# Performance work log

Hardware: AMD Instinct MI355X
Metric: run time of the kernel (lower is better)

## Reference

```python
import jax, jax.numpy as jnp
import numpy as np

N_MELS, HIDDEN, HEAD_DIM = 80, 128, 64


def _gru_step(h, gx_t, w_hh, b_hh):
    # PyTorch GRU cell math. gx_t = x_t @ W_ih^T + b_ih, precomputed. [B, 3H]
    H = h.shape[-1]
    gh = h @ w_hh.T + b_hh  # [B, 3H]
    r = jax.nn.sigmoid(gx_t[:, :H] + gh[:, :H])
    z = jax.nn.sigmoid(gx_t[:, H:2 * H] + gh[:, H:2 * H])
    n = jnp.tanh(gx_t[:, 2 * H:] + r * gh[:, 2 * H:])
    return (1.0 - z) * n + z * h


def setup_inputs() -> dict:
    key = jax.random.key(0)
    ks = jax.random.split(key, 14)
    s = 1.0 / np.sqrt(HIDDEN)
    u = lambda k, shape, sc: jax.random.uniform(k, shape, jnp.float32, -sc, sc)
    return {
        "x": jax.random.normal(ks[0], (128, 1500, N_MELS), dtype=jnp.float32),
        # forward-direction GRU params
        "w_ih_f": u(ks[1], (3 * HIDDEN, N_MELS), s),
        "w_hh_f": u(ks[2], (3 * HIDDEN, HIDDEN), s),
        "b_ih_f": u(ks[3], (3 * HIDDEN,), s),
        "b_hh_f": u(ks[4], (3 * HIDDEN,), s),
        # backward-direction GRU params
        "w_ih_b": u(ks[5], (3 * HIDDEN, N_MELS), s),
        "w_hh_b": u(ks[6], (3 * HIDDEN, HIDDEN), s),
        "b_ih_b": u(ks[7], (3 * HIDDEN,), s),
        "b_hh_b": u(ks[8], (3 * HIDDEN,), s),
        # MLP head: Linear(2H, 64) -> ReLU -> Linear(64, 1)
        "w1": u(ks[9], (HEAD_DIM, 2 * HIDDEN), 1.0 / np.sqrt(2 * HIDDEN)),
        "b1": u(ks[10], (HEAD_DIM,), 1.0 / np.sqrt(2 * HIDDEN)),
        "w2": u(ks[11], (1, HEAD_DIM), 1.0 / np.sqrt(HEAD_DIM)),
        "b2": u(ks[12], (1,), 1.0 / np.sqrt(HEAD_DIM)),
    }


def reference(x, w_ih_f, w_hh_f, b_ih_f, b_hh_f, w_ih_b, w_hh_b, b_ih_b, b_hh_b, w1, b1, w2, b2):
    B, T, _ = x.shape
    h0 = jnp.zeros((B, HIDDEN), dtype=x.dtype)

    # Forward direction: last output = final hidden state after full scan.
    # Precompute input projections for all timesteps in one GEMM.
    gx_f = jnp.einsum('bti,gi->tbg', x, w_ih_f) + b_ih_f  # [T, B, 3H]
    h_f, _ = jax.lax.scan(lambda h, g: (_gru_step(h, g, w_hh_f, b_hh_f), None), h0, gx_f)

    # Backward direction: out[:, -1, H:] in PyTorch is the backward hidden
    # after processing ONLY x[:, -1] (the reverse scan's first step), so a
    # single GRU step from h0 reproduces it exactly.
    gx_b_last = x[:, -1, :] @ w_ih_b.T + b_ih_b  # [B, 3H]
    h_b = _gru_step(h0, gx_b_last, w_hh_b, b_hh_b)

    last = jnp.concatenate([h_f, h_b], axis=-1)  # [B, 2H]
    # Head (eval mode: dropout is identity)
    hdn = jax.nn.relu(last @ w1.T + b1)
    out = hdn @ w2.T + b2  # [B, 1]
    return out[:, 0]
```

## Files before the change

kernel.cpp:

```cpp
#include <hip/hip_runtime.h>

#define B 128
#define T 1500
#define NI 80
#define H 128
#define G 384
#define TT 64

typedef float v2f __attribute__((ext_vector_type(2)));

__device__ __forceinline__ float sigf(float x) { return 1.0f / (1.0f + __expf(-x)); }
__device__ __forceinline__ float tanhfast(float x) { return 1.0f - 2.0f / (1.0f + __expf(2.0f * x)); }
__device__ __forceinline__ v2f pkfma(v2f a, v2f b, v2f c) { return __builtin_elementwise_fma(a, b, c); }

__device__ __forceinline__ float sum8(float v) {
    int a = __builtin_bit_cast(int, v);
    float m = __builtin_bit_cast(float, __builtin_amdgcn_update_dpp(0, a, 0x141, 0xF, 0xF, true));
    float s = v + m;
    a = __builtin_bit_cast(int, s);
    m = __builtin_bit_cast(float, __builtin_amdgcn_update_dpp(0, a, 0x1B, 0xF, 0xF, true));
    s = s + m;
    a = __builtin_bit_cast(int, s);
    m = __builtin_bit_cast(float, __builtin_amdgcn_update_dpp(0, a, 0xB1, 0xF, 0xF, true));
    return s + m;
}

__global__ __launch_bounds__(384)
void gx_gemm_kernel(const float* __restrict__ x, const float* __restrict__ w_ih,
                    const float* __restrict__ b_ih, float* __restrict__ gx,
                    int t0, int ct) {
    int tile = blockIdx.x;
    int b = blockIdx.y;
    int tl0 = tile * TT;
    if (tl0 >= ct) return;
    int n = (ct - tl0 < TT) ? (ct - tl0) : TT;
    int tid = threadIdx.x;

    __shared__ __align__(16) float xs[TT * NI];
    const float4* xsrc4 = (const float4*)(x + ((size_t)b * T + (size_t)(t0 + tl0)) * NI);
    int total4 = n * (NI / 4);
    for (int i = tid; i < total4; i += 384) ((float4*)xs)[i] = xsrc4[i];

    v2f w2[40];
    const v2f* wr = (const v2f*)(w_ih + (size_t)tid * NI);
#pragma unroll
    for (int i = 0; i < 40; ++i) w2[i] = wr[i];
    float bias = b_ih[tid];
    __syncthreads();

    float* gout = gx + ((size_t)b * ct + (size_t)tl0) * G + tid;
    int tt = 0;
    for (; tt + 2 <= n; tt += 2) {
        const float4* xa4 = (const float4*)(xs + tt * NI);
        const float4* xb4 = (const float4*)(xs + (tt + 1) * NI);
        v2f a0 = {0.f, 0.f}, a1 = {0.f, 0.f}, c0 = {0.f, 0.f}, c1 = {0.f, 0.f};
#pragma unroll
        for (int i = 0; i < 20; ++i) {
            float4 xa = xa4[i];
            float4 xb = xb4[i];
            v2f alo = {xa.x, xa.y}, ahi = {xa.z, xa.w};
            v2f blo = {xb.x, xb.y}, bhi = {xb.z, xb.w};
            a0 = pkfma(w2[2 * i], alo, a0);
            a1 = pkfma(w2[2 * i + 1], ahi, a1);
            c0 = pkfma(w2[2 * i], blo, c0);
            c1 = pkfma(w2[2 * i + 1], bhi, c1);
        }
        gout[(size_t)tt * G]       = bias + ((a0.x + a0.y) + (a1.x + a1.y));
        gout[(size_t)(tt + 1) * G] = bias + ((c0.x + c0.y) + (c1.x + c1.y));
    }
    if (tt < n) {
        const float4* xa4 = (const float4*)(xs + tt * NI);
        v2f a0 = {0.f, 0.f}, a1 = {0.f, 0.f};
#pragma unroll
        for (int i = 0; i < 20; ++i) {
            float4 xa = xa4[i];
            v2f alo = {xa.x, xa.y}, ahi = {xa.z, xa.w};
            a0 = pkfma(w2[2 * i], alo, a0);
            a1 = pkfma(w2[2 * i + 1], ahi, a1);
        }
        gout[(size_t)tt * G] = bias + ((a0.x + a0.y) + (a1.x + a1.y));
    }
}

__global__ __launch_bounds__(512)
void scan_kernel(const float* __restrict__ gx, const float* __restrict__ w_hh,
                 const float* __restrict__ b_hh, float* __restrict__ h_state,
                 int ct, int first, int last,
                 const float* __restrict__ x,
                 const float* __restrict__ w_ih_b, const float* __restrict__ b_ih_b,
                 const float* __restrict__ b_hh_b,
                 const float* __restrict__ w1, const float* __restrict__ b1,
                 const float* __restrict__ w2, const float* __restrict__ b2,
                 float* __restrict__ out) {
    int b = blockIdx.x;
    int tid = threadIdx.x;
    int jp = tid >> 3;
    int q = tid & 7;
    int j0 = jp, j1 = jp + 64;
    int jsel = (q < 4) ? j0 : j1;
    int hsel = ((jsel >> 4) * 20) + (jsel & 15);
    bool writer = (q & 3) == 0;

    __shared__ __align__(16) float hs[2][160];
    __shared__ __align__(16) float tail_gx[G];
    __shared__ __align__(16) float last_s[2 * H];
    __shared__ __align__(16) float xb_s[NI];

    float4 W0r[4], W0z[4], W0n[4], W1r[4], W1z[4], W1n[4];
    {
        const float* wb = w_hh + 16 * q;
        const float4* p0 = (const float4*)(wb + (size_t)j0 * H);
        const float4* p1 = (const float4*)(wb + (size_t)(j0 + H) * H);
        const float4* p2 = (const float4*)(wb + (size_t)(j0 + 2 * H) * H);
        const float4* p3 = (const float4*)(wb + (size_t)j1 * H);
        const float4* p4 = (const float4*)(wb + (size_t)(j1 + H) * H);
        const float4* p5 = (const float4*)(wb + (size_t)(j1 + 2 * H) * H);
#pragma unroll
        for (int i = 0; i < 4; ++i) {
            W0r[i] = p0[i]; W0z[i] = p1[i]; W0n[i] = p2[i];
            W1r[i] = p3[i]; W1z[i] = p4[i]; W1n[i] = p5[i];
        }
    }
    float br = b_hh[jsel], bz = b_hh[jsel + H], bn = b_hh[jsel + 2 * H];

    float h_cur = 0.f;
    if (!first) h_cur = h_state[b * H + jsel];
    if (writer) hs[0][hsel] = h_cur;

    float ga0, ga1, ga2, gb0 = 0.f, gb1 = 0.f, gb2 = 0.f;
    {
        const float* gp = gx + (size_t)b * ct * G;
        ga0 = gp[jsel]; ga1 = gp[jsel + H]; ga2 = gp[jsel + 2 * H];
        if (ct > 1) { gb0 = gp[G + jsel]; gb1 = gp[G + jsel + H]; gb2 = gp[G + jsel + 2 * H]; }
    }
    __syncthreads();

    auto step = [&](int TL, int SB, float& g0, float& g1, float& g2) {
        const float4* hv4 = (const float4*)(&hs[SB][0] + 20 * q);
        float4 h0 = hv4[0], h1 = hv4[1], h2 = hv4[2], h3 = hv4[3];
        v2f a0r = {0.f, 0.f}, a0z = {0.f, 0.f}, a0n = {0.f, 0.f};
        v2f a1r = {0.f, 0.f}, a1z = {0.f, 0.f}, a1n = {0.f, 0.f};
        v2f hl, hh;
        hl = v2f{h0.x, h0.y}; hh = v2f{h0.z, h0.w};
        a0r = pkfma(v2f{W0r[0].x, W0r[0].y}, hl, a0r); a0r = pkfma(v2f{W0r[0].z, W0r[0].w}, hh, a0r);
        a0z = pkfma(v2f{W0z[0].x, W0z[0].y}, hl, a0z); a0z = pkfma(v2f{W0z[0].z, W0z[0].w}, hh, a0z);
        a0n = pkfma(v2f{W0n[0].x, W0n[0].y}, hl, a0n); a0n = pkfma(v2f{W0n[0].z, W0n[0].w}, hh, a0n);
        a1r = pkfma(v2f{W1r[0].x, W1r[0].y}, hl, a1r); a1r = pkfma(v2f{W1r[0].z, W1r[0].w}, hh, a1r);
        a1z = pkfma(v2f{W1z[0].x, W1z[0].y}, hl, a1z); a1z = pkfma(v2f{W1z[0].z, W1z[0].w}, hh, a1z);
        a1n = pkfma(v2f{W1n[0].x, W1n[0].y}, hl, a1n); a1n = pkfma(v2f{W1n[0].z, W1n[0].w}, hh, a1n);
        hl = v2f{h1.x, h1.y}; hh = v2f{h1.z, h1.w};
        a0r = pkfma(v2f{W0r[1].x, W0r[1].y}, hl, a0r); a0r = pkfma(v2f{W0r[1].z, W0r[1].w}, hh, a0r);
        a0z = pkfma(v2f{W0z[1].x, W0z[1].y}, hl, a0z); a0z = pkfma(v2f{W0z[1].z, W0z[1].w}, hh, a0z);
        a0n = pkfma(v2f{W0n[1].x, W0n[1].y}, hl, a0n); a0n = pkfma(v2f{W0n[1].z, W0n[1].w}, hh, a0n);
        a1r = pkfma(v2f{W1r[1].x, W1r[1].y}, hl, a1r); a1r = pkfma(v2f{W1r[1].z, W1r[1].w}, hh, a1r);
        a1z = pkfma(v2f{W1z[1].x, W1z[1].y}, hl, a1z); a1z = pkfma(v2f{W1z[1].z, W1z[1].w}, hh, a1z);
        a1n = pkfma(v2f{W1n[1].x, W1n[1].y}, hl, a1n); a1n = pkfma(v2f{W1n[1].z, W1n[1].w}, hh, a1n);
        hl = v2f{h2.x, h2.y}; hh = v2f{h2.z, h2.w};
        a0r = pkfma(v2f{W0r[2].x, W0r[2].y}, hl, a0r); a0r = pkfma(v2f{W0r[2].z, W0r[2].w}, hh, a0r);
        a0z = pkfma(v2f{W0z[2].x, W0z[2].y}, hl, a0z); a0z = pkfma(v2f{W0z[2].z, W0z[2].w}, hh, a0z);
        a0n = pkfma(v2f{W0n[2].x, W0n[2].y}, hl, a0n); a0n = pkfma(v2f{W0n[2].z, W0n[2].w}, hh, a0n);
        a1r = pkfma(v2f{W1r[2].x, W1r[2].y}, hl, a1r); a1r = pkfma(v2f{W1r[2].z, W1r[2].w}, hh, a1r);
        a1z = pkfma(v2f{W1z[2].x, W1z[2].y}, hl, a1z); a1z = pkfma(v2f{W1z[2].z, W1z[2].w}, hh, a1z);
        a1n = pkfma(v2f{W1n[2].x, W1n[2].y}, hl, a1n); a1n = pkfma(v2f{W1n[2].z, W1n[2].w}, hh, a1n);
        hl = v2f{h3.x, h3.y}; hh = v2f{h3.z, h3.w};
        a0r = pkfma(v2f{W0r[3].x, W0r[3].y}, hl, a0r); a0r = pkfma(v2f{W0r[3].z, W0r[3].w}, hh, a0r);
        a0z = pkfma(v2f{W0z[3].x, W0z[3].y}, hl, a0z); a0z = pkfma(v2f{W0z[3].z, W0z[3].w}, hh, a0z);
        a0n = pkfma(v2f{W0n[3].x, W0n[3].y}, hl, a0n); a0n = pkfma(v2f{W0n[3].z, W0n[3].w}, hh, a0n);
        a1r = pkfma(v2f{W1r[3].x, W1r[3].y}, hl, a1r); a1r = pkfma(v2f{W1r[3].z, W1r[3].w}, hh, a1r);
        a1z = pkfma(v2f{W1z[3].x, W1z[3].y}, hl, a1z); a1z = pkfma(v2f{W1z[3].z, W1z[3].w}, hh, a1z);
        a1n = pkfma(v2f{W1n[3].x, W1n[3].y}, hl, a1n); a1n = pkfma(v2f{W1n[3].z, W1n[3].w}, hh, a1n);

        float s0r = sum8(a0r.x + a0r.y), s0z = sum8(a0z.x + a0z.y), s0n = sum8(a0n.x + a0n.y);
        float s1r = sum8(a1r.x + a1r.y), s1z = sum8(a1z.x + a1z.y), s1n = sum8(a1n.x + a1n.y);
        bool lo = q < 4;
        float ar = lo ? s0r : s1r;
        float az = lo ? s0z : s1z;
        float an = lo ? s0n : s1n;
        float r = sigf(g0 + br + ar);
        float z = sigf(g1 + bz + az);
        float n = tanhfast(g2 + r * (bn + an));
        h_cur = n + z * (h_cur - n);
        if (writer) hs[SB ^ 1][hsel] = h_cur;
        if (TL + 2 < ct) {
            const float* gp = gx + ((size_t)b * ct + TL + 2) * G;
            g0 = gp[jsel]; g1 = gp[jsel + H]; g2 = gp[jsel + 2 * H];
        }
        asm volatile("s_waitcnt lgkmcnt(0)\n\ts_barrier" ::: "memory");
    };

    int tl = 0;
    for (; tl + 1 < ct; tl += 2) {
        step(tl,     0, ga0, ga1, ga2);
        step(tl + 1, 1, gb0, gb1, gb2);
    }
    if (tl < ct) step(tl, 0, ga0, ga1, ga2);

    if (!last) {
        if (writer) h_state[b * H + jsel] = h_cur;
        return;
    }

    if (tid < NI) xb_s[tid] = x[((size_t)b * T + (T - 1)) * NI + tid];
    if (writer) last_s[jsel] = h_cur;
    __syncthreads();

    if (tid < G) {
        const float4* wbr = (const float4*)(w_ih_b + (size_t)tid * NI);
        const float4* xv = (const float4*)xb_s;
        float a0 = 0.f, a1 = 0.f, a2 = 0.f, a3 = 0.f;
#pragma unroll
        for (int i = 0; i < 20; ++i) {
            float4 wv = wbr[i]; float4 x4 = xv[i];
            a0 = fmaf(wv.x, x4.x, a0); a1 = fmaf(wv.y, x4.y, a1);
            a2 = fmaf(wv.z, x4.z, a2); a3 = fmaf(wv.w, x4.w, a3);
        }
        tail_gx[tid] = b_ih_b[tid] + ((a0 + a1) + (a2 + a3));
    }
    __syncthreads();

    if (tid < H) {
        float r = sigf(tail_gx[tid] + b_hh_b[tid]);
        float z = sigf(tail_gx[tid + H] + b_hh_b[tid + H]);
        float n = tanhfast(tail_gx[tid + 2 * H] + r * b_hh_b[tid + 2 * H]);
        last_s[H + tid] = (1.f - z) * n;
    }
    __syncthreads();

    if (tid < 64) {
        const float4* w1r = (const float4*)(w1 + (size_t)tid * 2 * H);
        const float4* lv = (const float4*)last_s;
        float a0 = 0.f, a1 = 0.f, a2 = 0.f, a3 = 0.f;
#pragma unroll
        for (int i = 0; i < 64; ++i) {
            float4 wv = w1r[i]; float4 l4 = lv[i];
            a0 = fmaf(wv.x, l4.x, a0); a1 = fmaf(wv.y, l4.y, a1);
            a2 = fmaf(wv.z, l4.z, a2); a3 = fmaf(wv.w, l4.w, a3);
        }
        float v = b1[tid] + ((a0 + a1) + (a2 + a3));
        v = fmaxf(v, 0.f) * w2[tid];
#pragma unroll
        for (int off = 32; off > 0; off >>= 1) v += __shfl_down(v, off);
        if (tid == 0) out[b] = v + b2[0];
    }
}

extern "C" void kernel_launch(void* const* d_in, const int* in_sizes, int n_in,
                              void* d_out, int out_size, void* d_ws, size_t ws_size,
                              hipStream_t stream) {
    (void)in_sizes; (void)n_in; (void)out_size;
    const float* x      = (const float*)d_in[0];
    const float* w_ih_f = (const float*)d_in[1];
    const float* w_hh_f = (const float*)d_in[2];
    const float* b_ih_f = (const float*)d_in[3];
    const float* b_hh_f = (const float*)d_in[4];
    const float* w_ih_b = (const float*)d_in[5];
    const float* w_hh_b = (const float*)d_in[6];
    const float* b_ih_b = (const float*)d_in[7];
    const float* b_hh_b = (const float*)d_in[8];
    const float* w1     = (const float*)d_in[9];
    const float* b1     = (const float*)d_in[10];
    const float* w2     = (const float*)d_in[11];
    const float* b2     = (const float*)d_in[12];
    (void)w_hh_b;
    float* out = (float*)d_out;

    float* h_state = (float*)d_ws;
    float* gxbuf = h_state + B * H;
    size_t hbytes = (size_t)B * H * sizeof(float);
    size_t avail = ws_size > hbytes ? ws_size - hbytes : 0;
    long long chunkT = (long long)(avail / ((size_t)B * G * sizeof(float)));
    if (chunkT > T) chunkT = T;
    if (chunkT < 1) chunkT = 1;

    for (int t0 = 0; t0 < T; t0 += (int)chunkT) {
        int ct = (T - t0 < (int)chunkT) ? (T - t0) : (int)chunkT;
        int ntiles = (ct + TT - 1) / TT;
        gx_gemm_kernel<<<dim3(ntiles, B), dim3(384), 0, stream>>>(
            x, w_ih_f, b_ih_f, gxbuf, t0, ct);
        scan_kernel<<<dim3(B), dim3(512), 0, stream>>>(
            gxbuf, w_hh_f, b_hh_f, h_state, ct,
            (t0 == 0) ? 1 : 0, (t0 + ct >= T) ? 1 : 0,
            x, w_ih_b, b_ih_b, b_hh_b, w1, b1, w2, b2, out);
    }
}
```

Before: 1.151 ms.

## Transpose gate-projection buffer, register-tile GEMM, prefetch four scan steps per load

The input-projection GEMM now writes gates as [B][G][T] instead of [B][T][G]. It is rewritten as a shared-memory tiled outer product: 64 gates by 128 timesteps per block, with each thread holding 4x8 accumulators. With the new layout the recurrent scan can fetch four consecutive timesteps per gate in one float4 load, prefetched a superstep ahead, which takes global loads off most serial steps. This requires chunk lengths to be multiples of 4, with clamped tail reads. It also adds register pressure from the launch-bounds occupancy hints.

Measured after the change: 1.209 ms. 5.0% more time.

```diff
diff --git a/kernel.cpp b/kernel.cpp
--- a/kernel.cpp
+++ b/kernel.cpp
@@ -5,7 +5,8 @@
 #define NI 80
 #define H 128
 #define G 384
-#define TT 64
+#define GT 64
+#define NTT 128
 
 typedef float v2f __attribute__((ext_vector_type(2)));
 
@@ -25,65 +26,81 @@
     return s + m;
 }
 
-__global__ __launch_bounds__(384)
+__global__ __launch_bounds__(256, 2)
 void gx_gemm_kernel(const float* __restrict__ x, const float* __restrict__ w_ih,
-                    const float* __restrict__ b_ih, float* __restrict__ gx,
+                    const float* __restrict__ b_ih, float* __restrict__ gxT,
                     int t0, int ct) {
-    int tile = blockIdx.x;
-    int b = blockIdx.y;
-    int tl0 = tile * TT;
-    if (tl0 >= ct) return;
-    int n = (ct - tl0 < TT) ? (ct - tl0) : TT;
+    __shared__ __align__(16) float wT[80][GT + 2];
+    __shared__ __align__(16) float xT[80][NTT + 4];
+    __shared__ float bias_s[GT];
     int tid = threadIdx.x;
-
-    __shared__ __align__(16) float xs[TT * NI];
-    const float4* xsrc4 = (const float4*)(x + ((size_t)b * T + (size_t)(t0 + tl0)) * NI);
-    int total4 = n * (NI / 4);
-    for (int i = tid; i < total4; i += 384) ((float4*)xs)[i] = xsrc4[i];
-
-    v2f w2[40];
-    const v2f* wr = (const v2f*)(w_ih + (size_t)tid * NI);
-#pragma unroll
-    for (int i = 0; i < 40; ++i) w2[i] = wr[i];
-    float bias = b_ih[tid];
-    __syncthreads();
-
-    float* gout = gx + ((size_t)b * ct + (size_t)tl0) * G + tid;
-    int tt = 0;
-    for (; tt + 2 <= n; tt += 2) {
-        const float4* xa4 = (const float4*)(xs + tt * NI);
-        const float4* xb4 = (const float4*)(xs + (tt + 1) * NI);
-        v2f a0 = {0.f, 0.f}, a1 = {0.f, 0.f}, c0 = {0.f, 0.f}, c1 = {0.f, 0.f};
-#pragma unroll
-        for (int i = 0; i < 20; ++i) {
-            float4 xa = xa4[i];
-            float4 xb = xb4[i];
-            v2f alo = {xa.x, xa.y}, ahi = {xa.z, xa.w};
-            v2f blo = {xb.x, xb.y}, bhi = {xb.z, xb.w};
-            a0 = pkfma(w2[2 * i], alo, a0);
-            a1 = pkfma(w2[2 * i + 1], ahi, a1);
-            c0 = pkfma(w2[2 * i], blo, c0);
-            c1 = pkfma(w2[2 * i + 1], bhi, c1);
-        }
-        gout[(size_t)tt * G]       = bias + ((a0.x + a0.y) + (a1.x + a1.y));
-        gout[(size_t)(tt + 1) * G] = bias + ((c0.x + c0.y) + (c1.x + c1.y));
-    }
-    if (tt < n) {
-        const float4* xa4 = (const float4*)(xs + tt * NI);
-        v2f a0 = {0.f, 0.f}, a1 = {0.f, 0.f};
-#pragma unroll
-        for (int i = 0; i < 20; ++i) {
-            float4 xa = xa4[i];
-            v2f alo = {xa.x, xa.y}, ahi = {xa.z, xa.w};
-            a0 = pkfma(w2[2 * i], alo, a0);
-            a1 = pkfma(w2[2 * i + 1], ahi, a1);
-        }
-        gout[(size_t)tt * G] = bias + ((a0.x + a0.y) + (a1.x + a1.y));
-    }
-}
-
-__global__ __launch_bounds__(512)
-void scan_kernel(const float* __restrict__ gx, const float* __restrict__ w_hh,
+    int b = blockIdx.z;
+    int g0b = blockIdx.y * GT;
+    int tt0 = blockIdx.x * NTT;
+
+    for (int i = tid; i < GT * 20; i += 256) {
+        int g = i & (GT - 1);
+        int kc = i >> 6;
+        float4 v = *(const float4*)(w_ih + (size_t)(g0b + g) * NI + 4 * kc);
+        wT[4 * kc + 0][g] = v.x; wT[4 * kc + 1][g] = v.y;
+        wT[4 * kc + 2][g] = v.z; wT[4 * kc + 3][g] = v.w;
+    }
+    for (int i = tid; i < NTT * 20; i += 256) {
+        int c = i & (NTT - 1);
+        int kc = i >> 7;
+        int tt = tt0 + c; if (tt > ct - 1) tt = ct - 1;
+        float4 v = *(const float4*)(x + ((size_t)b * T + (size_t)(t0 + tt)) * NI + 4 * kc);
+        xT[4 * kc + 0][c] = v.x; xT[4 * kc + 1][c] = v.y;
+        xT[4 * kc + 2][c] = v.z; xT[4 * kc + 3][c] = v.w;
+    }
+    if (tid < GT) bias_s[tid] = b_ih[g0b + tid];
+    __syncthreads();
+
+    int gi = tid & 15;
+    int ti = tid >> 4;
+    v2f acc[4][4];
+#pragma unroll
+    for (int r = 0; r < 4; ++r)
+#pragma unroll
+        for (int j = 0; j < 4; ++j) acc[r][j] = v2f{0.f, 0.f};
+
+#pragma unroll 2
+    for (int k = 0; k < 80; ++k) {
+        const v2f* wv = (const v2f*)&wT[k][4 * gi];
+        v2f w01 = wv[0], w23 = wv[1];
+        const float4* xv = (const float4*)&xT[k][8 * ti];
+        float4 x03 = xv[0], x47 = xv[1];
+        v2f xp0 = {x03.x, x03.y}, xp1 = {x03.z, x03.w};
+        v2f xp2 = {x47.x, x47.y}, xp3 = {x47.z, x47.w};
+        float wr[4] = {w01.x, w01.y, w23.x, w23.y};
+#pragma unroll
+        for (int r = 0; r < 4; ++r) {
+            v2f ws = {wr[r], wr[r]};
+            acc[r][0] = pkfma(ws, xp0, acc[r][0]);
+            acc[r][1] = pkfma(ws, xp1, acc[r][1]);
+            acc[r][2] = pkfma(ws, xp2, acc[r][2]);
+            acc[r][3] = pkfma(ws, xp3, acc[r][3]);
+        }
+    }
+
+#pragma unroll
+    for (int r = 0; r < 4; ++r) {
+        int g = g0b + 4 * gi + r;
+        float bias = bias_s[4 * gi + r];
+        float* orow = gxT + ((size_t)b * G + g) * ct + tt0 + 8 * ti;
+#pragma unroll
+        for (int j = 0; j < 4; ++j) {
+            int t = tt0 + 8 * ti + 2 * j;
+            if (t < ct) {
+                float2 o; o.x = acc[r][j].x + bias; o.y = acc[r][j].y + bias;
+                *(float2*)(orow + 2 * j) = o;
+            }
+        }
+    }
+}
+
+__global__ __launch_bounds__(512, 2)
+void scan_kernel(const float* __restrict__ gxT, const float* __restrict__ w_hh,
                  const float* __restrict__ b_hh, float* __restrict__ h_state,
                  int ct, int first, int last,
                  const float* __restrict__ x,
@@ -106,17 +123,17 @@
     __shared__ __align__(16) float last_s[2 * H];
     __shared__ __align__(16) float xb_s[NI];
 
-    float4 W0r[4], W0z[4], W0n[4], W1r[4], W1z[4], W1n[4];
+    v2f W0r[8], W0z[8], W0n[8], W1r[8], W1z[8], W1n[8];
     {
         const float* wb = w_hh + 16 * q;
-        const float4* p0 = (const float4*)(wb + (size_t)j0 * H);
-        const float4* p1 = (const float4*)(wb + (size_t)(j0 + H) * H);
-        const float4* p2 = (const float4*)(wb + (size_t)(j0 + 2 * H) * H);
-        const float4* p3 = (const float4*)(wb + (size_t)j1 * H);
-        const float4* p4 = (const float4*)(wb + (size_t)(j1 + H) * H);
-        const float4* p5 = (const float4*)(wb + (size_t)(j1 + 2 * H) * H);
-#pragma unroll
-        for (int i = 0; i < 4; ++i) {
+        const v2f* p0 = (const v2f*)(wb + (size_t)j0 * H);
+        const v2f* p1 = (const v2f*)(wb + (size_t)(j0 + H) * H);
+        const v2f* p2 = (const v2f*)(wb + (size_t)(j0 + 2 * H) * H);
+        const v2f* p3 = (const v2f*)(wb + (size_t)j1 * H);
+        const v2f* p4 = (const v2f*)(wb + (size_t)(j1 + H) * H);
+        const v2f* p5 = (const v2f*)(wb + (size_t)(j1 + 2 * H) * H);
+#pragma unroll
+        for (int i = 0; i < 8; ++i) {
             W0r[i] = p0[i]; W0z[i] = p1[i]; W0n[i] = p2[i];
             W1r[i] = p3[i]; W1z[i] = p4[i]; W1n[i] = p5[i];
         }
@@ -127,49 +144,34 @@
     if (!first) h_cur = h_state[b * H + jsel];
     if (writer) hs[0][hsel] = h_cur;
 
-    float ga0, ga1, ga2, gb0 = 0.f, gb1 = 0.f, gb2 = 0.f;
+    const float* gp0 = gxT + ((size_t)b * G + jsel) * ct;
+    const float* gp1 = gp0 + (size_t)H * ct;
+    const float* gp2 = gp0 + (size_t)(2 * H) * ct;
+
+    float4 A0, A1, A2, B0, B1, B2;
+    A0 = *(const float4*)(gp0); A1 = *(const float4*)(gp1); A2 = *(const float4*)(gp2);
     {
-        const float* gp = gx + (size_t)b * ct * G;
-        ga0 = gp[jsel]; ga1 = gp[jsel + H]; ga2 = gp[jsel + 2 * H];
-        if (ct > 1) { gb0 = gp[G + jsel]; gb1 = gp[G + jsel + H]; gb2 = gp[G + jsel + 2 * H]; }
-    }
-    __syncthreads();
-
-    auto step = [&](int TL, int SB, float& g0, float& g1, float& g2) {
-        const float4* hv4 = (const float4*)(&hs[SB][0] + 20 * q);
+        int t4 = (ct - 4 < 4) ? (ct - 4) : 4;
+        B0 = *(const float4*)(gp0 + t4); B1 = *(const float4*)(gp1 + t4); B2 = *(const float4*)(gp2 + t4);
+    }
+    __syncthreads();
+
+    auto dostep = [&](float g0, float g1, float g2, const float* SRC, float* DST) {
+        const float4* hv4 = (const float4*)(SRC + 20 * q);
         float4 h0 = hv4[0], h1 = hv4[1], h2 = hv4[2], h3 = hv4[3];
         v2f a0r = {0.f, 0.f}, a0z = {0.f, 0.f}, a0n = {0.f, 0.f};
         v2f a1r = {0.f, 0.f}, a1z = {0.f, 0.f}, a1n = {0.f, 0.f};
-        v2f hl, hh;
-        hl = v2f{h0.x, h0.y}; hh = v2f{h0.z, h0.w};
-        a0r = pkfma(v2f{W0r[0].x, W0r[0].y}, hl, a0r); a0r = pkfma(v2f{W0r[0].z, W0r[0].w}, hh, a0r);
-        a0z = pkfma(v2f{W0z[0].x, W0z[0].y}, hl, a0z); a0z = pkfma(v2f{W0z[0].z, W0z[0].w}, hh, a0z);
-        a0n = pkfma(v2f{W0n[0].x, W0n[0].y}, hl, a0n); a0n = pkfma(v2f{W0n[0].z, W0n[0].w}, hh, a0n);
-        a1r = pkfma(v2f{W1r[0].x, W1r[0].y}, hl, a1r); a1r = pkfma(v2f{W1r[0].z, W1r[0].w}, hh, a1r);
-        a1z = pkfma(v2f{W1z[0].x, W1z[0].y}, hl, a1z); a1z = pkfma(v2f{W1z[0].z, W1z[0].w}, hh, a1z);
-        a1n = pkfma(v2f{W1n[0].x, W1n[0].y}, hl, a1n); a1n = pkfma(v2f{W1n[0].z, W1n[0].w}, hh, a1n);
-        hl = v2f{h1.x, h1.y}; hh = v2f{h1.z, h1.w};
-        a0r = pkfma(v2f{W0r[1].x, W0r[1].y}, hl, a0r); a0r = pkfma(v2f{W0r[1].z, W0r[1].w}, hh, a0r);
-        a0z = pkfma(v2f{W0z[1].x, W0z[1].y}, hl, a0z); a0z = pkfma(v2f{W0z[1].z, W0z[1].w}, hh, a0z);
-        a0n = pkfma(v2f{W0n[1].x, W0n[1].y}, hl, a0n); a0n = pkfma(v2f{W0n[1].z, W0n[1].w}, hh, a0n);
-        a1r = pkfma(v2f{W1r[1].x, W1r[1].y}, hl, a1r); a1r = pkfma(v2f{W1r[1].z, W1r[1].w}, hh, a1r);
-        a1z = pkfma(v2f{W1z[1].x, W1z[1].y}, hl, a1z); a1z = pkfma(v2f{W1z[1].z, W1z[1].w}, hh, a1z);
-        a1n = pkfma(v2f{W1n[1].x, W1n[1].y}, hl, a1n); a1n = pkfma(v2f{W1n[1].z, W1n[1].w}, hh, a1n);
-        hl = v2f{h2.x, h2.y}; hh = v2f{h2.z, h2.w};
-        a0r = pkfma(v2f{W0r[2].x, W0r[2].y}, hl, a0r); a0r = pkfma(v2f{W0r[2].z, W0r[2].w}, hh, a0r);
-        a0z = pkfma(v2f{W0z[2].x, W0z[2].y}, hl, a0z); a0z = pkfma(v2f{W0z[2].z, W0z[2].w}, hh, a0z);
-        a0n = pkfma(v2f{W0n[2].x, W0n[2].y}, hl, a0n); a0n = pkfma(v2f{W0n[2].z, W0n[2].w}, hh, a0n);
-        a1r = pkfma(v2f{W1r[2].x, W1r[2].y}, hl, a1r); a1r = pkfma(v2f{W1r[2].z, W1r[2].w}, hh, a1r);
-        a1z = pkfma(v2f{W1z[2].x, W1z[2].y}, hl, a1z); a1z = pkfma(v2f{W1z[2].z, W1z[2].w}, hh, a1z);
-        a1n = pkfma(v2f{W1n[2].x, W1n[2].y}, hl, a1n); a1n = pkfma(v2f{W1n[2].z, W1n[2].w}, hh, a1n);
-        hl = v2f{h3.x, h3.y}; hh = v2f{h3.z, h3.w};
-        a0r = pkfma(v2f{W0r[3].x, W0r[3].y}, hl, a0r); a0r = pkfma(v2f{W0r[3].z, W0r[3].w}, hh, a0r);
-        a0z = pkfma(v2f{W0z[3].x, W0z[3].y}, hl, a0z); a0z = pkfma(v2f{W0z[3].z, W0z[3].w}, hh, a0z);
-        a0n = pkfma(v2f{W0n[3].x, W0n[3].y}, hl, a0n); a0n = pkfma(v2f{W0n[3].z, W0n[3].w}, hh, a0n);
-        a1r = pkfma(v2f{W1r[3].x, W1r[3].y}, hl, a1r); a1r = pkfma(v2f{W1r[3].z, W1r[3].w}, hh, a1r);
-        a1z = pkfma(v2f{W1z[3].x, W1z[3].y}, hl, a1z); a1z = pkfma(v2f{W1z[3].z, W1z[3].w}, hh, a1z);
-        a1n = pkfma(v2f{W1n[3].x, W1n[3].y}, hl, a1n); a1n = pkfma(v2f{W1n[3].z, W1n[3].w}, hh, a1n);
-
+        float4 hh[4] = {h0, h1, h2, h3};
+#pragma unroll
+        for (int i = 0; i < 4; ++i) {
+            v2f hl = {hh[i].x, hh[i].y}, hg = {hh[i].z, hh[i].w};
+            a0r = pkfma(W0r[2 * i], hl, a0r); a0r = pkfma(W0r[2 * i + 1], hg, a0r);
+            a0z = pkfma(W0z[2 * i], hl, a0z); a0z = pkfma(W0z[2 * i + 1], hg, a0z);
+            a0n = pkfma(W0n[2 * i], hl, a0n); a0n = pkfma(W0n[2 * i + 1], hg, a0n);
+            a1r = pkfma(W1r[2 * i], hl, a1r); a1r = pkfma(W1r[2 * i + 1], hg, a1r);
+            a1z = pkfma(W1z[2 * i], hl, a1z); a1z = pkfma(W1z[2 * i + 1], hg, a1z);
+            a1n = pkfma(W1n[2 * i], hl, a1n); a1n = pkfma(W1n[2 * i + 1], hg, a1n);
+        }
         float s0r = sum8(a0r.x + a0r.y), s0z = sum8(a0z.x + a0z.y), s0n = sum8(a0n.x + a0n.y);
         float s1r = sum8(a1r.x + a1r.y), s1z = sum8(a1z.x + a1z.y), s1n = sum8(a1n.x + a1n.y);
         bool lo = q < 4;
@@ -180,20 +182,30 @@
         float z = sigf(g1 + bz + az);
         float n = tanhfast(g2 + r * (bn + an));
         h_cur = n + z * (h_cur - n);
-        if (writer) hs[SB ^ 1][hsel] = h_cur;
-        if (TL + 2 < ct) {
-            const float* gp = gx + ((size_t)b * ct + TL + 2) * G;
-            g0 = gp[jsel]; g1 = gp[jsel + H]; g2 = gp[jsel + 2 * H];
-        }
+        if (writer) DST[hsel] = h_cur;
         asm volatile("s_waitcnt lgkmcnt(0)\n\ts_barrier" ::: "memory");
     };
 
+    auto superstep = [&](int TL, float4& S0, float4& S1, float4& S2) {
+        float l00 = S0.x, l01 = S0.y, l02 = S0.z, l03 = S0.w;
+        float l10 = S1.x, l11 = S1.y, l12 = S1.z, l13 = S1.w;
+        float l20 = S2.x, l21 = S2.y, l22 = S2.z, l23 = S2.w;
+        int tpf = TL + 8; if (tpf > ct - 4) tpf = ct - 4;
+        S0 = *(const float4*)(gp0 + tpf);
+        S1 = *(const float4*)(gp1 + tpf);
+        S2 = *(const float4*)(gp2 + tpf);
+        dostep(l00, l10, l20, hs[0], hs[1]);
+        dostep(l01, l11, l21, hs[1], hs[0]);
+        dostep(l02, l12, l22, hs[0], hs[1]);
+        dostep(l03, l13, l23, hs[1], hs[0]);
+    };
+
     int tl = 0;
-    for (; tl + 1 < ct; tl += 2) {
-        step(tl,     0, ga0, ga1, ga2);
-        step(tl + 1, 1, gb0, gb1, gb2);
-    }
-    if (tl < ct) step(tl, 0, ga0, ga1, ga2);
+    for (; tl + 8 <= ct; tl += 8) {
+        superstep(tl, A0, A1, A2);
+        superstep(tl + 4, B0, B1, B2);
+    }
+    if (tl < ct) superstep(tl, A0, A1, A2);
 
     if (!last) {
         if (writer) h_state[b * H + jsel] = h_cur;
@@ -269,13 +281,14 @@
     size_t hbytes = (size_t)B * H * sizeof(float);
     size_t avail = ws_size > hbytes ? ws_size - hbytes : 0;
     long long chunkT = (long long)(avail / ((size_t)B * G * sizeof(float)));
+    chunkT &= ~3LL;
     if (chunkT > T) chunkT = T;
-    if (chunkT < 1) chunkT = 1;
+    if (chunkT < 4) chunkT = 4;
 
     for (int t0 = 0; t0 < T; t0 += (int)chunkT) {
         int ct = (T - t0 < (int)chunkT) ? (T - t0) : (int)chunkT;
-        int ntiles = (ct + TT - 1) / TT;
-        gx_gemm_kernel<<<dim3(ntiles, B), dim3(384), 0, stream>>>(
+        int ttiles = (ct + NTT - 1) / NTT;
+        gx_gemm_kernel<<<dim3(ttiles, G / GT, B), dim3(256), 0, stream>>>(
             x, w_ih_f, b_ih_f, gxbuf, t0, ct);
         scan_kernel<<<dim3(B), dim3(512), 0, stream>>>(
             gxbuf, w_hh_f, b_hh_f, h_state, ct,
```
